# Kernel tuning notes

Hardware: AMD Instinct MI355X
Metric: run time of the kernel (lower is better)

Reference implementation:

```python
import jax, jax.numpy as jnp
import numpy as np

L = 512       # sequence length
N_AA = 21     # amino-acid alphabet size
D = 128       # per-residue substitution embedding dim
N1 = 256
N2 = 256


def setup_inputs() -> dict:
    key = jax.random.key(0)
    k1, k2, k3 = jax.random.split(key, 3)
    X1 = jax.random.randint(k1, (N1, L), 0, N_AA)
    X2 = jax.random.randint(k2, (N2, L), 0, N_AA)
    W = jax.random.normal(k3, (L * N_AA, N_AA * D), dtype=jnp.float32) * 0.02
    b = jnp.zeros((N_AA * D,), jnp.float32)
    w_param = jnp.zeros((L * (L - 1) // 2,), jnp.float32)
    a = jnp.ones((1,), jnp.float32)
    return {"X1": X1, "X2": X2, "W": W, "b": b, "w_param": w_param, "a": a}


def _network(X, W, b):
    # one-hot + linear stand-in for self.network; outputs (n, n_aa, d)
    n = X.shape[0]
    oh = jax.nn.one_hot(X, N_AA, dtype=W.dtype).reshape(n, -1)  # (n, L*n_aa)
    return (oh @ W + b).reshape(n, N_AA, -1)


def _wdk(subs, w):
    # torch: (subs[:, graph] * w).sum(2) * subs, summed over dim 1
    # graph[i] = arange(L), so this equals subs @ w^T contracted with subs:
    # out[..] = sum_i sum_j subs[.., i] * w[i, j] * subs[.., j]
    return jnp.einsum('...i,ij,...j->...', subs, w, subs)


def reference(X1, X2, W, b, w_param, a):
    n1, Lx = X1.shape
    n2 = X2.shape[0]

    # symmetric pairwise weight matrix; diagonal stays 0 -> sigmoid(0)=0.5
    i_x, i_y = np.tril_indices(Lx, k=-1)
    wm = jnp.zeros((Lx, Lx), W.dtype).at[i_x, i_y].set(w_param).at[i_y, i_x].set(w_param)
    w = jax.nn.sigmoid(wm)

    # per-sequence substitution matrices S = E E^T, (n, n_aa, n_aa)
    E1 = _network(X1, W, b)
    S1 = jnp.einsum('nad,nbd->nab', E1, E1)
    E2 = _network(X2, W, b)
    S2 = jnp.einsum('nad,nbd->nab', E2, E2)

    r1 = jnp.arange(n1)
    r2 = jnp.arange(n2)

    # self terms: subs[n, l] = S[n, X[n,l], X[n,l]]
    d1 = S1[r1[:, None], X1, X1]                  # (n1, L)
    k1 = _wdk(d1, w)[:, None]                     # (n1, 1)
    d2 = S2[r2[:, None], X2, X2]                  # (n2, L)
    k2 = _wdk(d2, w)[None, :]                     # (1, n2)

    # cross terms: average of the two sequences' S, gathered directly
    # (avoids materializing the (n1*n2, n_aa, n_aa) averaged S tensor)
    g1 = S1[r1[:, None, None], X1[:, None, :], X2[None, :, :]]  # (n1, n2, L)
    g2 = S2[r2[None, :, None], X1[:, None, :], X2[None, :, :]]  # (n1, n2, L)
    subs = 0.5 * (g1 + g2)

    K = _wdk(subs, w)                             # (n1, n2)
    K = K / jnp.sqrt(k1) / jnp.sqrt(k2)
    return (a ** 2) * K
```

## Files before the change

kernel.cpp:

```cpp
#include <hip/hip_runtime.h>
#include <cstdint>
#include <cstddef>

typedef __attribute__((ext_vector_type(8))) __bf16 bf16x8;
typedef __attribute__((ext_vector_type(4))) float f32x4;
typedef __attribute__((ext_vector_type(16))) float f32x16;

__device__ __forceinline__ unsigned short f2b(float x) {
    uint32_t u = __float_as_uint(x);
    u += 0x7FFFu + ((u >> 16) & 1u);
    return (unsigned short)(u >> 16);
}
__device__ __forceinline__ float b2f(unsigned short h) {
    return __uint_as_float(((uint32_t)h) << 16);
}

__device__ __forceinline__ void gl16(const unsigned short* g, unsigned short* l) {
    __builtin_amdgcn_global_load_lds((const __attribute__((address_space(1))) uint32_t*)g,
                                     (__attribute__((address_space(3))) uint32_t*)l, 16, 0, 0);
}

#define L_SEQ 512
#define N_AA 21
#define DDIM 128
#define NCOL 2688
#define NSEQ 512
#define TBSTRIDE 448
#define KTOT 10752
#define ZCH 12
#define KBTOT 672
#define KBCH 56

#define PB_WBZ   2688
#define PB_REPACK 1024
#define PB_WBUILD 1024
#define PB_ABZ   2688
#define PB_TOTAL (PB_WBZ + PB_REPACK + PB_WBUILD + PB_ABZ)

#define WS_PAD 684

__global__ __launch_bounds__(256) void prep_kernel(const int* X1, const int* X2,
                                                   const float* W, const float* wp,
                                                   uint8_t* X8,
                                                   float* w32, unsigned short* wswz,
                                                   unsigned short* Wbz, unsigned short* Abz) {
    __shared__ unsigned short Ws[16 * WS_PAD];
    int bid = blockIdx.x;
    int t = threadIdx.x;
    if (bid < PB_WBZ) {
        int kb = bid >> 2, cw = bid & 3;
        int r0 = kb * 16, c0 = cw * 672;
        for (int e = t; e < 16 * 168; e += 256) {
            int ri = e / 168, c4 = e - ri * 168;
            float4 v = *(const float4*)(W + (size_t)(r0 + ri) * NCOL + c0 + c4 * 4);
            union { ushort4 q; unsigned short s[4]; } o;
            o.s[0] = f2b(v.x); o.s[1] = f2b(v.y); o.s[2] = f2b(v.z); o.s[3] = f2b(v.w);
            *(ushort4*)&Ws[ri * WS_PAD + c4 * 4] = o.q;
        }
        __syncthreads();
        for (int e = t; e < 21 * 64; e += 256) {
            int fi = e >> 6, sl = e & 63;
            int lr = sl & 31, hf = sl >> 5;
            union { uint4 q; unsigned short s[8]; } o;
#pragma unroll
            for (int j = 0; j < 8; ++j) o.s[j] = Ws[(hf * 8 + j) * WS_PAD + fi * 32 + lr];
            int cb = cw * 21 + fi;
            *(uint4*)&Wbz[((size_t)cb * KBTOT + kb) * 512 + sl * 8] = o.q;
        }
        return;
    }
    bid -= PB_WBZ;
    if (bid < PB_REPACK) {
        int e = bid * 256 + t;
        if (e < 131072) X8[e] = (uint8_t)X1[e];
        else            X8[e] = (uint8_t)X2[e - 131072];
        return;
    }
    bid -= PB_REPACK;
    if (bid < PB_WBUILD) {
        int e = bid * 256 + t;
        int p = e >> 9, q = e & 511;
        float x = 0.0f;
        if (p > q)      x = wp[p * (p - 1) / 2 + q];
        else if (p < q) x = wp[q * (q - 1) / 2 + p];
        float s = 1.0f / (1.0f + expf(-x));
        w32[e] = s;
        int nb = p >> 5, lr = p & 31;
        int kb = q >> 4, hf = (q >> 3) & 1, j = q & 7;
        wswz[(size_t)((nb * 32 + kb) * 512) + (hf * 32 + lr) * 8 + j] = f2b(s);
        return;
    }
    bid -= PB_WBUILD;
    {
        int f = bid * 4 + (t >> 6);
        int lane = t & 63, lr = lane & 31, hf = lane >> 5;
        int mb = f / KBTOT, kb = f - mb * KBTOT;
        int m = mb * 32 + lr;
        const int* Xrow = (m < 256) ? (X1 + (size_t)m * L_SEQ) : (X2 + (size_t)(m - 256) * L_SEQ);
        int k0 = kb * 16 + hf * 8;
        union { uint4 q; unsigned short s[8]; } o;
#pragma unroll
        for (int j = 0; j < 8; ++j) {
            int k = k0 + j;
            int l = k / N_AA;
            int aa = k - l * N_AA;
            o.s[j] = (Xrow[l] == aa) ? (unsigned short)0x3F80u : (unsigned short)0u;
        }
        *(uint4*)&Abz[(size_t)f * 512 + lane * 8] = o.q;
    }
}

__global__ __launch_bounds__(256, 4) void e_mfma_v6(const unsigned short* Abz, const unsigned short* Wbz, float* Ep) {
    __shared__ unsigned short lds[4 * 8 * 512];

    int lin = blockIdx.x;
    int s = ((lin & 7) * 126) + (lin >> 3);
    int cx = s % 21;
    int rem = s / 21;
    int my = rem & 3;
    int kz = rem >> 2;

    int t = threadIdx.x, wid = t >> 6, lane = t & 63;
    int lr = lane & 31, hf = lane >> 5;
    int kb0 = kz * KBCH;

    const unsigned short* Aw = Abz + ((size_t)((my * 4 + wid) * KBTOT + kb0)) * 512 + lane * 8;
    const unsigned short* Bw = Wbz + ((size_t)((cx * 4 + wid) * KBTOT + kb0)) * 512 + lane * 8;
    unsigned short* La = &lds[wid * 512];
    unsigned short* Lb = &lds[(4 + wid) * 512];

#define STG(buf_, kb_) do { \
        gl16(Aw + (size_t)(kb_) * 512, La + (buf_) * 4096); \
        gl16(Bw + (size_t)(kb_) * 512, Lb + (buf_) * 4096); \
    } while (0)

    int alo = (wid & 1) * 2;
    int blo = 4 + (wid >> 1) * 2;

    f32x16 acc00, acc01, acc10, acc11;
#pragma unroll
    for (int r = 0; r < 16; ++r) { acc00[r] = 0.f; acc01[r] = 0.f; acc10[r] = 0.f; acc11[r] = 0.f; }

#define COMPUTE(kb_) do { \
        const unsigned short* base = &lds[((kb_) & 3) * 4096]; \
        bf16x8 a0 = *(const bf16x8*)(base + (alo + 0) * 512 + lane * 8); \
        bf16x8 a1 = *(const bf16x8*)(base + (alo + 1) * 512 + lane * 8); \
        bf16x8 b0 = *(const bf16x8*)(base + (blo + 0) * 512 + lane * 8); \
        bf16x8 b1 = *(const bf16x8*)(base + (blo + 1) * 512 + lane * 8); \
        acc00 = __builtin_amdgcn_mfma_f32_32x32x16_bf16(a0, b0, acc00, 0, 0, 0); \
        acc01 = __builtin_amdgcn_mfma_f32_32x32x16_bf16(a0, b1, acc01, 0, 0, 0); \
        acc10 = __builtin_amdgcn_mfma_f32_32x32x16_bf16(a1, b0, acc10, 0, 0, 0); \
        acc11 = __builtin_amdgcn_mfma_f32_32x32x16_bf16(a1, b1, acc11, 0, 0, 0); \
    } while (0)

    STG(0, 0); STG(1, 1); STG(2, 2);

#pragma unroll 1
    for (int kb = 0; kb < KBCH - 3; ++kb) {
        asm volatile("s_waitcnt vmcnt(4)" ::: "memory");
        __builtin_amdgcn_s_barrier();
        __builtin_amdgcn_sched_barrier(0);
        STG((kb + 3) & 3, kb + 3);
        COMPUTE(kb);
    }
    asm volatile("s_waitcnt vmcnt(4)" ::: "memory");
    __builtin_amdgcn_s_barrier();
    __builtin_amdgcn_sched_barrier(0);
    COMPUTE(KBCH - 3);
    asm volatile("s_waitcnt vmcnt(2)" ::: "memory");
    __builtin_amdgcn_s_barrier();
    __builtin_amdgcn_sched_barrier(0);
    COMPUTE(KBCH - 2);
    asm volatile("s_waitcnt vmcnt(0)" ::: "memory");
    __builtin_amdgcn_s_barrier();
    __builtin_amdgcn_sched_barrier(0);
    COMPUTE(KBCH - 1);

#undef STG
#undef COMPUTE

    int mb0 = my * 4 + (wid & 1) * 2;
    int cb0 = cx * 4 + (wid >> 1) * 2;
    float* slab = Ep + (size_t)kz * NSEQ * NCOL;
#pragma unroll
    for (int r = 0; r < 16; ++r) {
        int row = (r & 3) + 8 * (r >> 2) + 4 * hf;
        float* base = slab + (size_t)(mb0 * 32 + row) * NCOL + cb0 * 32 + lr;
        base[0] = acc00[r];
        base[32] = acc01[r];
        base[(size_t)32 * NCOL] = acc10[r];
        base[(size_t)32 * NCOL + 32] = acc11[r];
    }
}

__global__ __launch_bounds__(256) void t_kernel(const float* Ep, const float* bvec,
                                                unsigned short* Tb, float* Tdiag) {
    __shared__ float4 Es4[21 * 33];
    int t = threadIdx.x, n = blockIdx.x;
    for (int idx = t; idx < 672; idx += 256) {
        const float4* bp = (const float4*)(bvec + idx * 4);
        float4 acc = *bp;
#pragma unroll
        for (int z = 0; z < ZCH; ++z) {
            float4 v = *(const float4*)(Ep + ((size_t)z * NSEQ + n) * NCOL + idx * 4);
            acc.x += v.x; acc.y += v.y; acc.z += v.z; acc.w += v.w;
        }
        int r = idx >> 5, d = idx & 31;
        Es4[r * 33 + d] = acc;
    }
    __syncthreads();
    for (int e = t; e < 441; e += 256) {
        int r = e / 21, c = e - r * 21;
        const float4* ar = &Es4[r * 33];
        const float4* br = &Es4[c * 33];
        float s = 0.f;
#pragma unroll 8
        for (int d = 0; d < 32; ++d) {
            float4 a = ar[d], b = br[d];
            s += a.x * b.x + a.y * b.y + a.z * b.z + a.w * b.w;
        }
        Tb[(size_t)n * TBSTRIDE + e] = f2b(0.5f * s);
        if (r == c) Tdiag[n * 24 + r] = s;
    }
}

__global__ __launch_bounds__(512) void k_kernel(const uint8_t* X8, const float* Tdiag, const float* w32, float* kinv) {
    __shared__ __align__(16) float dvec[4][512];
    __shared__ float Td[4][21];
    __shared__ float wred[4][8];
    int t = threadIdx.x, n0 = blockIdx.x * 4;
    if (t < 84) Td[t / 21][t % 21] = Tdiag[(size_t)(n0 + t / 21) * 24 + (t % 21)];
    __syncthreads();
    for (int e = t; e < 2048; e += 512) {
        int nn = e >> 9, l = e & 511;
        dvec[nn][l] = Td[nn][X8[(size_t)(n0 + nn) * 512 + l]];
    }
    __syncthreads();
    int wid = t >> 6, lane = t & 63;
    int q0 = lane * 8;

    float4 dA0 = *(const float4*)&dvec[0][q0], dA1 = *(const float4*)&dvec[0][q0 + 4];
    float4 dB0 = *(const float4*)&dvec[1][q0], dB1 = *(const float4*)&dvec[1][q0 + 4];
    float4 dC0 = *(const float4*)&dvec[2][q0], dC1 = *(const float4*)&dvec[2][q0 + 4];
    float4 dD0 = *(const float4*)&dvec[3][q0], dD1 = *(const float4*)&dvec[3][q0 + 4];

    float4 rA0 = {0,0,0,0}, rA1 = {0,0,0,0}, rB0 = {0,0,0,0}, rB1 = {0,0,0,0};
    float4 rC0 = {0,0,0,0}, rC1 = {0,0,0,0}, rD0 = {0,0,0,0}, rD1 = {0,0,0,0};

#define FMA4(R, W, S) do { (R).x += (W).x * (S); (R).y += (W).y * (S); (R).z += (W).z * (S); (R).w += (W).w * (S); } while (0)
    for (int p = wid; p < 512; p += 8) {
        const float4* wr = (const float4*)(w32 + (size_t)p * 512 + q0);
        float4 w0v = wr[0], w1v = wr[1];
        float a = dvec[0][p], b = dvec[1][p], c = dvec[2][p], d = dvec[3][p];
        FMA4(rA0, w0v, a); FMA4(rA1, w1v, a);
        FMA4(rB0, w0v, b); FMA4(rB1, w1v, b);
        FMA4(rC0, w0v, c); FMA4(rC1, w1v, c);
        FMA4(rD0, w0v, d); FMA4(rD1, w1v, d);
    }
#undef FMA4

#define DOT8(R0, R1, D0, D1) ((R0).x*(D0).x + (R0).y*(D0).y + (R0).z*(D0).z + (R0).w*(D0).w + \
                              (R1).x*(D1).x + (R1).y*(D1).y + (R1).z*(D1).z + (R1).w*(D1).w)
    float s0 = DOT8(rA0, rA1, dA0, dA1);
    float s1 = DOT8(rB0, rB1, dB0, dB1);
    float s2 = DOT8(rC0, rC1, dC0, dC1);
    float s3 = DOT8(rD0, rD1, dD0, dD1);
#undef DOT8

#pragma unroll
    for (int off = 1; off < 64; off <<= 1) {
        s0 += __shfl_xor(s0, off);
        s1 += __shfl_xor(s1, off);
        s2 += __shfl_xor(s2, off);
        s3 += __shfl_xor(s3, off);
    }
    if (lane == 0) { wred[0][wid] = s0; wred[1][wid] = s1; wred[2][wid] = s2; wred[3][wid] = s3; }
    __syncthreads();
    if (t < 4) {
        float kk = 0.f;
#pragma unroll
        for (int w = 0; w < 8; ++w) kk += wred[t][w];
        kinv[n0 + t] = 1.0f / sqrtf(kk);
    }
}

__global__ __launch_bounds__(512, 6) void k4_kernel(const uint8_t* X8, const unsigned short* Tb,
                                                    const unsigned short* wswz, const float* kinv,
                                                    const float* Ainp, float* out) {
    __shared__ unsigned short Sh[32 * 520];
    __shared__ unsigned short Ts1h[4 * TBSTRIDE];
    __shared__ unsigned short Ts2h[8 * TBSTRIDE];
    __shared__ unsigned short A21[4 * 512];
    __shared__ uint8_t Xs2[8 * 512];
    __shared__ float Kacc[8][32];

    int t = threadIdx.x;
    int i0 = blockIdx.x * 4;
    int j0 = blockIdx.y * 8;

    for (int e = t; e < 4 * 512; e += 512)
        A21[e] = (unsigned short)(21 * X8[(size_t)(i0 + (e >> 9)) * 512 + (e & 511)]);
    {
        const uint32_t* s2 = (const uint32_t*)(X8 + (size_t)(256 + j0) * 512);
        uint32_t* d2 = (uint32_t*)Xs2;
        for (int e = t; e < 1024; e += 512) d2[e] = s2[e];
    }
    {
        uint32_t* d1 = (uint32_t*)Ts1h;
        for (int e = t; e < 4 * 224; e += 512) {
            int r = e / 224, w = e - r * 224;
            d1[e] = ((const uint32_t*)(Tb + (size_t)(i0 + r) * TBSTRIDE))[w];
        }
        uint32_t* d2 = (uint32_t*)Ts2h;
        for (int e = t; e < 8 * 224; e += 512) {
            int r = e / 224, w = e - r * 224;
            d2[e] = ((const uint32_t*)(Tb + (size_t)(256 + j0 + r) * TBSTRIDE))[w];
        }
    }
    __syncthreads();

    for (int e4 = t; e4 < 32 * 128; e4 += 512) {
        int pr = e4 >> 7, p = (e4 & 127) * 4;
        int ti = pr >> 3, tj = pr & 7;
        uint64_t a4 = *(const uint64_t*)&A21[ti * 512 + p];
        uint32_t b4 = *(const uint32_t*)&Xs2[tj * 512 + p];
        const unsigned short* T1 = &Ts1h[ti * TBSTRIDE];
        const unsigned short* T2 = &Ts2h[tj * TBSTRIDE];
        uint64_t outw = 0;
#pragma unroll
        for (int u = 0; u < 4; ++u) {
            int idx = (int)((a4 >> (16 * u)) & 0xFFFFu) + (int)((b4 >> (8 * u)) & 0xFFu);
            float v = b2f(T1[idx]) + b2f(T2[idx]);
            outw |= (uint64_t)f2b(v) << (16 * u);
        }
        *(uint64_t*)&Sh[pr * 520 + p] = outw;
    }
    __syncthreads();

    int wid = t >> 6, lane = t & 63;
    int lr = lane & 31, hf = lane >> 5;
    int n_base = wid * 64;

    const unsigned short* Sa = &Sh[lr * 520 + hf * 8];
    const unsigned short* Bz0 = wswz + (size_t)((wid * 2 + 0) * 32) * 512 + lane * 8;
    const unsigned short* Bz1 = wswz + (size_t)((wid * 2 + 1) * 32) * 512 + lane * 8;

    f32x16 acc0, acc1;
#pragma unroll
    for (int j = 0; j < 16; ++j) { acc0[j] = 0.f; acc1[j] = 0.f; }

#pragma unroll 2
    for (int kt = 0; kt < 32; ++kt) {
        bf16x8 av = *(const bf16x8*)(Sa + kt * 16);
        bf16x8 bv0 = *(const bf16x8*)(Bz0 + kt * 512);
        bf16x8 bv1 = *(const bf16x8*)(Bz1 + kt * 512);
        acc0 = __builtin_amdgcn_mfma_f32_32x32x16_bf16(av, bv0, acc0, 0, 0, 0);
        acc1 = __builtin_amdgcn_mfma_f32_32x32x16_bf16(av, bv1, acc1, 0, 0, 0);
    }

    float prow[16];
#pragma unroll
    for (int r = 0; r < 16; ++r) {
        int row = (r & 3) + 8 * (r >> 2) + 4 * hf;
        float v = acc0[r] * b2f(Sh[row * 520 + (n_base + lr)]);
        v      += acc1[r] * b2f(Sh[row * 520 + (n_base + 32 + lr)]);
        prow[r] = v;
    }
#pragma unroll
    for (int r = 0; r < 16; ++r) {
        float v = prow[r];
        v += __shfl_xor(v, 1);
        v += __shfl_xor(v, 2);
        v += __shfl_xor(v, 4);
        v += __shfl_xor(v, 8);
        v += __shfl_xor(v, 16);
        if (lr == 0) {
            int row = (r & 3) + 8 * (r >> 2) + 4 * hf;
            Kacc[wid][row] = v;
        }
    }
    __syncthreads();

    if (t < 32) {
        float K = Kacc[0][t] + Kacc[1][t] + Kacc[2][t] + Kacc[3][t]
                + Kacc[4][t] + Kacc[5][t] + Kacc[6][t] + Kacc[7][t];
        int ti = t >> 3, tj = t & 7;
        int i = i0 + ti, j = j0 + tj;
        float a0 = Ainp[0];
        out[i * 256 + j] = a0 * a0 * K * kinv[i] * kinv[256 + j];
    }
}

extern "C" void kernel_launch(void* const* d_in, const int* in_sizes, int n_in,
                              void* d_out, int out_size, void* d_ws, size_t ws_size,
                              hipStream_t stream) {
    const int*   X1 = (const int*)d_in[0];
    const int*   X2 = (const int*)d_in[1];
    const float* W  = (const float*)d_in[2];
    const float* b  = (const float*)d_in[3];
    const float* wp = (const float*)d_in[4];
    const float* a  = (const float*)d_in[5];
    float* out = (float*)d_out;

    char* ws = (char*)d_ws;
    unsigned short* Tb    = (unsigned short*)(ws + 0);
    float*          Tdiag = (float*)(ws + 458752);
    float*          w32   = (float*)(ws + 507904);
    unsigned short* wswz  = (unsigned short*)(ws + 1556480);
    float*          kinv  = (float*)(ws + 2080768);
    uint8_t*        X8    = (uint8_t*)(ws + 2082816);
    unsigned short* Abz   = (unsigned short*)(ws + 2344960);
    unsigned short* Wbz   = (unsigned short*)(ws + 13355008);
    float*          Ep    = (float*)(ws + 71157760);

    prep_kernel<<<PB_TOTAL, 256, 0, stream>>>(X1, X2, W, wp, X8, w32, wswz, Wbz, Abz);
    e_mfma_v6<<<1008, 256, 0, stream>>>(Abz, Wbz, Ep);
    t_kernel<<<512, 256, 0, stream>>>(Ep, b, Tb, Tdiag);
    k_kernel<<<128, 512, 0, stream>>>(X8, Tdiag, w32, kinv);
    k4_kernel<<<dim3(64, 32), 512, 0, stream>>>(X8, Tb, wswz, kinv, a, out);
}
```

Before: 327.7 us.

## Enlarge k4 tile to 4x16 pairs with 1024-thread blocks sharing w fragments

The cross-kernel block now handles 64 sequence pairs (4x16) with 16 waves instead of 32 pairs with 8 waves. Each wave loads one w fragment column block and reuses it across two 32-row A tiles, which halves global w traffic per pair and halves the grid size. The Sh row padding changes from 520 to 516. The larger block raises LDS and register pressure per block, may lower occupancy, and the new padding may change LDS bank conflicts.

```diff
diff --git a/kernel.cpp b/kernel.cpp
--- a/kernel.cpp
+++ b/kernel.cpp
@@ -38,6 +38,7 @@
 #define PB_TOTAL (PB_WBZ + PB_REPACK + PB_WBUILD + PB_ABZ)
 
 #define WS_PAD 684
+#define SH_PAD 516
 
 __global__ __launch_bounds__(256) void prep_kernel(const int* X1, const int* X2,
                                                    const float* W, const float* wp,
@@ -284,44 +285,44 @@
     }
 }
 
-__global__ __launch_bounds__(512, 6) void k4_kernel(const uint8_t* X8, const unsigned short* Tb,
-                                                    const unsigned short* wswz, const float* kinv,
-                                                    const float* Ainp, float* out) {
-    __shared__ unsigned short Sh[32 * 520];
+__global__ __launch_bounds__(1024, 4) void k4_kernel(const uint8_t* X8, const unsigned short* Tb,
+                                                     const unsigned short* wswz, const float* kinv,
+                                                     const float* Ainp, float* out) {
+    __shared__ unsigned short Sh[64 * SH_PAD];
     __shared__ unsigned short Ts1h[4 * TBSTRIDE];
-    __shared__ unsigned short Ts2h[8 * TBSTRIDE];
+    __shared__ unsigned short Ts2h[16 * TBSTRIDE];
     __shared__ unsigned short A21[4 * 512];
-    __shared__ uint8_t Xs2[8 * 512];
-    __shared__ float Kacc[8][32];
+    __shared__ uint8_t Xs2[16 * 512];
+    __shared__ float Kacc[16][64];
 
     int t = threadIdx.x;
     int i0 = blockIdx.x * 4;
-    int j0 = blockIdx.y * 8;
-
-    for (int e = t; e < 4 * 512; e += 512)
+    int j0 = blockIdx.y * 16;
+
+    for (int e = t; e < 4 * 512; e += 1024)
         A21[e] = (unsigned short)(21 * X8[(size_t)(i0 + (e >> 9)) * 512 + (e & 511)]);
     {
         const uint32_t* s2 = (const uint32_t*)(X8 + (size_t)(256 + j0) * 512);
         uint32_t* d2 = (uint32_t*)Xs2;
-        for (int e = t; e < 1024; e += 512) d2[e] = s2[e];
+        for (int e = t; e < 2048; e += 1024) d2[e] = s2[e];
     }
     {
         uint32_t* d1 = (uint32_t*)Ts1h;
-        for (int e = t; e < 4 * 224; e += 512) {
+        for (int e = t; e < 4 * 224; e += 1024) {
             int r = e / 224, w = e - r * 224;
             d1[e] = ((const uint32_t*)(Tb + (size_t)(i0 + r) * TBSTRIDE))[w];
         }
         uint32_t* d2 = (uint32_t*)Ts2h;
-        for (int e = t; e < 8 * 224; e += 512) {
+        for (int e = t; e < 16 * 224; e += 1024) {
             int r = e / 224, w = e - r * 224;
             d2[e] = ((const uint32_t*)(Tb + (size_t)(256 + j0 + r) * TBSTRIDE))[w];
         }
     }
     __syncthreads();
 
-    for (int e4 = t; e4 < 32 * 128; e4 += 512) {
+    for (int e4 = t; e4 < 64 * 128; e4 += 1024) {
         int pr = e4 >> 7, p = (e4 & 127) * 4;
-        int ti = pr >> 3, tj = pr & 7;
+        int ti = pr >> 4, tj = pr & 15;
         uint64_t a4 = *(const uint64_t*)&A21[ti * 512 + p];
         uint32_t b4 = *(const uint32_t*)&Xs2[tj * 512 + p];
         const unsigned short* T1 = &Ts1h[ti * TBSTRIDE];
@@ -333,17 +334,16 @@
             float v = b2f(T1[idx]) + b2f(T2[idx]);
             outw |= (uint64_t)f2b(v) << (16 * u);
         }
-        *(uint64_t*)&Sh[pr * 520 + p] = outw;
+        *(uint64_t*)&Sh[pr * SH_PAD + p] = outw;
     }
     __syncthreads();
 
     int wid = t >> 6, lane = t & 63;
     int lr = lane & 31, hf = lane >> 5;
-    int n_base = wid * 64;
-
-    const unsigned short* Sa = &Sh[lr * 520 + hf * 8];
-    const unsigned short* Bz0 = wswz + (size_t)((wid * 2 + 0) * 32) * 512 + lane * 8;
-    const unsigned short* Bz1 = wswz + (size_t)((wid * 2 + 1) * 32) * 512 + lane * 8;
+
+    const unsigned short* Sa0 = &Sh[lr * SH_PAD + hf * 8];
+    const unsigned short* Sa1 = Sa0 + 32 * SH_PAD;
+    const unsigned short* Bz = wswz + (size_t)(wid * 32) * 512 + lane * 8;
 
     f32x16 acc0, acc1;
 #pragma unroll
@@ -351,40 +351,35 @@
 
 #pragma unroll 2
     for (int kt = 0; kt < 32; ++kt) {
-        bf16x8 av = *(const bf16x8*)(Sa + kt * 16);
-        bf16x8 bv0 = *(const bf16x8*)(Bz0 + kt * 512);
-        bf16x8 bv1 = *(const bf16x8*)(Bz1 + kt * 512);
-        acc0 = __builtin_amdgcn_mfma_f32_32x32x16_bf16(av, bv0, acc0, 0, 0, 0);
-        acc1 = __builtin_amdgcn_mfma_f32_32x32x16_bf16(av, bv1, acc1, 0, 0, 0);
-    }
-
-    float prow[16];
+        bf16x8 bv  = *(const bf16x8*)(Bz + kt * 512);
+        bf16x8 av0 = *(const bf16x8*)(Sa0 + kt * 16);
+        bf16x8 av1 = *(const bf16x8*)(Sa1 + kt * 16);
+        acc0 = __builtin_amdgcn_mfma_f32_32x32x16_bf16(av0, bv, acc0, 0, 0, 0);
+        acc1 = __builtin_amdgcn_mfma_f32_32x32x16_bf16(av1, bv, acc1, 0, 0, 0);
+    }
+
 #pragma unroll
     for (int r = 0; r < 16; ++r) {
         int row = (r & 3) + 8 * (r >> 2) + 4 * hf;
-        float v = acc0[r] * b2f(Sh[row * 520 + (n_base + lr)]);
-        v      += acc1[r] * b2f(Sh[row * 520 + (n_base + 32 + lr)]);
-        prow[r] = v;
-    }
-#pragma unroll
-    for (int r = 0; r < 16; ++r) {
-        float v = prow[r];
-        v += __shfl_xor(v, 1);
-        v += __shfl_xor(v, 2);
-        v += __shfl_xor(v, 4);
-        v += __shfl_xor(v, 8);
-        v += __shfl_xor(v, 16);
+        float v0 = acc0[r] * b2f(Sh[row * SH_PAD + wid * 32 + lr]);
+        float v1 = acc1[r] * b2f(Sh[(row + 32) * SH_PAD + wid * 32 + lr]);
+        v0 += __shfl_xor(v0, 1);  v1 += __shfl_xor(v1, 1);
+        v0 += __shfl_xor(v0, 2);  v1 += __shfl_xor(v1, 2);
+        v0 += __shfl_xor(v0, 4);  v1 += __shfl_xor(v1, 4);
+        v0 += __shfl_xor(v0, 8);  v1 += __shfl_xor(v1, 8);
+        v0 += __shfl_xor(v0, 16); v1 += __shfl_xor(v1, 16);
         if (lr == 0) {
-            int row = (r & 3) + 8 * (r >> 2) + 4 * hf;
-            Kacc[wid][row] = v;
-        }
-    }
-    __syncthreads();
-
-    if (t < 32) {
-        float K = Kacc[0][t] + Kacc[1][t] + Kacc[2][t] + Kacc[3][t]
-                + Kacc[4][t] + Kacc[5][t] + Kacc[6][t] + Kacc[7][t];
-        int ti = t >> 3, tj = t & 7;
+            Kacc[wid][row] = v0;
+            Kacc[wid][32 + row] = v1;
+        }
+    }
+    __syncthreads();
+
+    if (t < 64) {
+        float K = 0.f;
+#pragma unroll
+        for (int w = 0; w < 16; ++w) K += Kacc[w][t];
+        int ti = t >> 4, tj = t & 15;
         int i = i0 + ti, j = j0 + tj;
         float a0 = Ainp[0];
         out[i * 256 + j] = a0 * a0 * K * kinv[i] * kinv[256 + j];
@@ -417,5 +412,5 @@
     e_mfma_v6<<<1008, 256, 0, stream>>>(Abz, Wbz, Ep);
     t_kernel<<<512, 256, 0, stream>>>(Ep, b, Tb, Tdiag);
     k_kernel<<<128, 512, 0, stream>>>(X8, Tdiag, w32, kinv);
-    k4_kernel<<<dim3(64, 32), 512, 0, stream>>>(X8, Tb, wswz, kinv, a, out);
-}
+    k4_kernel<<<dim3(64, 16), 1024, 0, stream>>>(X8, Tb, wswz, kinv, a, out);
+}
```

After: 439.5 us. +34.1%, slower.
